# Optimization experiments

Hardware: AMD Instinct MI355X
Metric: run time of the kernel (lower is better)

Reference implementation:

```python
import jax, jax.numpy as jnp
import numpy as np

B, C, L = 8, 256, 2048
D = C // 8  # q/k channel dim = 32


def setup_inputs() -> dict:
    key = jax.random.key(0)
    kx, kq, kk, kv, kg = jax.random.split(key, 5)
    kq1, kq2 = jax.random.split(kq)
    kk1, kk2 = jax.random.split(kk)
    kv1, kv2 = jax.random.split(kv)
    s = 0.05
    return {
        "x": jax.random.normal(kx, (B, C, L), dtype=jnp.float32),
        "Wq": jax.random.normal(kq1, (D, C), dtype=jnp.float32) * s,
        "bq": jax.random.normal(kq2, (D,), dtype=jnp.float32) * s,
        "Wk": jax.random.normal(kk1, (D, C), dtype=jnp.float32) * s,
        "bk": jax.random.normal(kk2, (D,), dtype=jnp.float32) * s,
        "Wv": jax.random.normal(kv1, (C, C), dtype=jnp.float32) * s,
        "bv": jax.random.normal(kv2, (C,), dtype=jnp.float32) * s,
        "gamma": jax.random.normal(kg, (1,), dtype=jnp.float32) * 0.1,
    }


def reference(x, Wq, bq, Wk, bk, Wv, bv, gamma):
    # 1x1 Conv1d == per-position channel matmul
    Q = jnp.einsum("dc,bcl->bld", Wq, x) + bq            # (B, L, D)
    K = jnp.einsum("dc,bcl->bdl", Wk, x) + bk[:, None]   # (B, D, L)
    V = jnp.einsum("oc,bcl->bol", Wv, x) + bv[:, None]   # (B, C, L)
    scale = jnp.float32(1.0 / np.sqrt(D))
    # attn[b, i, j]: softmax over j (keys)
    attn = jax.nn.softmax(jnp.einsum("bid,bdj->bij", Q, K) * scale, axis=-1)
    # out = V @ attn^T : out[b, c, i] = sum_j V[b, c, j] * attn[b, i, j]
    out = jnp.einsum("bcj,bij->bci", V, attn)            # (B, C, L)
    return gamma * out + x
```

## Files before the change

### kernel.cpp

```cpp
#include <hip/hip_runtime.h>
#include <stdint.h>


#define BB 8
#define CC 256
#define LL 2048
#define DD 32

typedef unsigned short u16;
typedef __attribute__((ext_vector_type(8))) short short8;
typedef __attribute__((ext_vector_type(4))) float f32x4;

#define SCALE_LOG2E 0.2550348612f

static __device__ __forceinline__ uint32_t pack2bf16(float hi, float lo) {
    return (__float_as_uint(hi) & 0xFFFF0000u) | (__float_as_uint(lo) >> 16);
}

static __device__ __forceinline__ float fexp2(float v) {
#if __has_builtin(__builtin_amdgcn_exp2f)
    return __builtin_amdgcn_exp2f(v);
#else
    return exp2f(v);
#endif
}

static __device__ __forceinline__ float frcp(float v) {
#if __has_builtin(__builtin_amdgcn_rcpf)
    return __builtin_amdgcn_rcpf(v);
#else
    return 1.0f / v;
#endif
}

__global__ __launch_bounds__(256) void prep_w_kernel(
    const float* __restrict__ Wq, const float* __restrict__ Wk,
    const float* __restrict__ Wv, u16* __restrict__ Wh)
{
    int idx = blockIdx.x * 256 + threadIdx.x;
    int r = idx >> 6;
    int c4 = (idx & 63) << 2;
    const float* src;
    if (r < 32)       src = Wq + (size_t)r * CC + c4;
    else if (r < 64)  src = Wk + (size_t)(r - 32) * CC + c4;
    else              src = Wv + (size_t)(r - 64) * CC + c4;
    float4 v = *(const float4*)src;
    uint2 o;
    o.x = pack2bf16(v.y, v.x);
    o.y = pack2bf16(v.w, v.z);
    *(uint2*)(Wh + (size_t)r * CC + c4) = o;
}

__global__ __launch_bounds__(512, 2) void proj_kernel(
    const float* __restrict__ x, const u16* __restrict__ Wh,
    const float* __restrict__ bq, const float* __restrict__ bk,
    const float* __restrict__ bv,
    u16* __restrict__ Qh, u16* __restrict__ Kth, u16* __restrict__ Vh)
{
    __shared__ u16 xls[32 * 264];
    const int blk = blockIdx.x;
    const int b = blk & 7;
    const int l0 = (blk >> 3) << 5;
    const int tid = threadIdx.x;
    const int w = tid >> 6;
    const int lane = tid & 63;
    const int ln = lane & 15;
    const int q = lane >> 4;

#pragma unroll
    for (int cc = 0; cc < 4; ++cc) {
        const int c = cc * 64 + (tid >> 3);
        const int l4 = (tid & 7) * 4;
        const float4 v = *(const float4*)(x + ((size_t)(b * CC + c)) * LL + l0 + l4);
        xls[(l4 + 0) * 264 + c] = (u16)(__float_as_uint(v.x) >> 16);
        xls[(l4 + 1) * 264 + c] = (u16)(__float_as_uint(v.y) >> 16);
        xls[(l4 + 2) * 264 + c] = (u16)(__float_as_uint(v.z) >> 16);
        xls[(l4 + 3) * 264 + c] = (u16)(__float_as_uint(v.w) >> 16);
    }
    __syncthreads();

    const int wl = w & 1;
    const int wm = w >> 1;
    const int mbase = wm * 80;
    const int l = l0 + wl * 16 + ln;

    f32x4 acc[5];
#pragma unroll
    for (int i = 0; i < 5; ++i) acc[i] = (f32x4){0.f, 0.f, 0.f, 0.f};

#pragma unroll
    for (int c0 = 0; c0 < CC; c0 += 32) {
        const short8 bf = *(const short8*)(&xls[(wl * 16 + ln) * 264 + c0 + q * 8]);
#pragma unroll
        for (int mt = 0; mt < 5; ++mt) {
            const short8 af = *(const short8*)(Wh + (size_t)(mbase + mt * 16 + ln) * CC + c0 + q * 8);
            acc[mt] = __builtin_amdgcn_mfma_f32_16x16x32_bf16(af, bf, acc[mt], 0, 0, 0);
        }
    }

#pragma unroll
    for (int mt = 0; mt < 5; ++mt) {
        const int rg = mbase + mt * 16 + q * 4;
        if (rg < 32) {
            float v0 = (acc[mt][0] + bq[rg + 0]) * SCALE_LOG2E;
            float v1 = (acc[mt][1] + bq[rg + 1]) * SCALE_LOG2E;
            float v2 = (acc[mt][2] + bq[rg + 2]) * SCALE_LOG2E;
            float v3 = (acc[mt][3] + bq[rg + 3]) * SCALE_LOG2E;
            uint2 o; o.x = pack2bf16(v1, v0); o.y = pack2bf16(v3, v2);
            *(uint2*)(Qh + ((size_t)(b * LL) + l) * DD + rg) = o;
        } else if (rg < 64) {
            const int rk = rg - 32;
            float v0 = acc[mt][0] + bk[rk + 0];
            float v1 = acc[mt][1] + bk[rk + 1];
            float v2 = acc[mt][2] + bk[rk + 2];
            float v3 = acc[mt][3] + bk[rk + 3];
            uint2 o; o.x = pack2bf16(v1, v0); o.y = pack2bf16(v3, v2);
            *(uint2*)(Kth + ((size_t)(b * LL) + l) * DD + rk) = o;
        } else {
            const int cv = rg - 64;
#pragma unroll
            for (int rr = 0; rr < 4; ++rr) {
                const float v = acc[mt][rr] + bv[cv + rr];
                Vh[((size_t)(b * CC) + cv + rr) * LL + l] = (u16)(__float_as_uint(v) >> 16);
            }
        }
    }
}

__global__ __launch_bounds__(512, 1) void attn_kernel(
    const u16* __restrict__ Qh, const u16* __restrict__ Kth,
    const u16* __restrict__ Vh, const float* __restrict__ x,
    const float* __restrict__ gamma, float* __restrict__ out)
{
    __shared__ u16 pbuf[8 * 64 * 40];
    __shared__ float obuf[256 * 68];
    __shared__ float lbuf[8 * 64];

    const int blk = blockIdx.x;
    const int b = blk & 7;
    const int i0 = (blk >> 3) << 6;
    const int tid = threadIdx.x;
    const int w = tid >> 6;
    const int wc = w >> 2;
    const int wj = w & 3;
    const int lane = tid & 63;
    const int ln = lane & 15;
    const int q = lane >> 4;

    u16* pb = pbuf + w * (64 * 40);
    const u16* Qb = Qh + ((size_t)(b * LL) + i0) * DD;
    const u16* Kb = Kth + (size_t)(b * LL) * DD;
    const u16* Vb = Vh + ((size_t)(b * CC) + wc * 128) * LL;

    short8 qf[4];
#pragma unroll
    for (int it = 0; it < 4; ++it)
        qf[it] = *(const short8*)(Qb + (size_t)(it * 16 + ln) * DD + q * 8);

    const f32x4 zf = {0.f, 0.f, 0.f, 0.f};
    f32x4 oacc[8][4];
#pragma unroll
    for (int a = 0; a < 8; ++a)
#pragma unroll
        for (int c = 0; c < 4; ++c) oacc[a][c] = zf;
    float lsum[4] = {0.f, 0.f, 0.f, 0.f};

    int jb = wj * 32;
    short8 kf0 = *(const short8*)(Kb + (size_t)(jb + ln) * DD + q * 8);
    short8 kf1 = *(const short8*)(Kb + (size_t)(jb + 16 + ln) * DD + q * 8);

    for (int n = 0; n < 16; ++n) {
        jb = n * 128 + wj * 32;
        const int jnx = (n < 15) ? (n + 1) * 128 + wj * 32 : jb;

        short8 vf[8];
#pragma unroll
        for (int ct = 0; ct < 8; ++ct)
            vf[ct] = *(const short8*)(Vb + (size_t)(ct * 16 + ln) * LL + jb + q * 8);
        const short8 kn0 = *(const short8*)(Kb + (size_t)(jnx + ln) * DD + q * 8);
        const short8 kn1 = *(const short8*)(Kb + (size_t)(jnx + 16 + ln) * DD + q * 8);

#pragma unroll
        for (int jt = 0; jt < 2; ++jt) {
            const short8 kf = jt ? kf1 : kf0;
#pragma unroll
            for (int it = 0; it < 4; ++it) {
                const f32x4 st = __builtin_amdgcn_mfma_f32_16x16x32_bf16(kf, qf[it], zf, 0, 0, 0);
                const float e0 = fexp2(st[0]), e1 = fexp2(st[1]);
                const float e2 = fexp2(st[2]), e3 = fexp2(st[3]);
                lsum[it] += (e0 + e1) + (e2 + e3);
                uint2 d; d.x = pack2bf16(e1, e0); d.y = pack2bf16(e3, e2);
                *(uint2*)(&pb[(it * 16 + ln) * 40 + jt * 16 + q * 4]) = d;
            }
        }

        short8 pf[4];
#pragma unroll
        for (int it = 0; it < 4; ++it)
            pf[it] = *(const short8*)(&pb[(it * 16 + ln) * 40 + q * 8]);

#pragma unroll
        for (int ct = 0; ct < 8; ++ct)
#pragma unroll
            for (int it = 0; it < 4; ++it)
                oacc[ct][it] = __builtin_amdgcn_mfma_f32_16x16x32_bf16(vf[ct], pf[it], oacc[ct][it], 0, 0, 0);

        kf0 = kn0; kf1 = kn1;
    }

#pragma unroll
    for (int it = 0; it < 4; ++it) {
        float s = lsum[it];
        s += __shfl_xor(s, 16);
        s += __shfl_xor(s, 32);
        lsum[it] = s;
    }
    if (q == 0) {
#pragma unroll
        for (int it = 0; it < 4; ++it) lbuf[w * 64 + it * 16 + ln] = lsum[it];
    }

#pragma unroll
    for (int p = 0; p < 4; ++p) {
        if (wj == p) {
#pragma unroll
            for (int ct = 0; ct < 8; ++ct)
#pragma unroll
                for (int it = 0; it < 4; ++it) {
                    const int i = it * 16 + ln;
#pragma unroll
                    for (int r = 0; r < 4; ++r) {
                        const int c = wc * 128 + ct * 16 + q * 4 + r;
                        if (p == 0) obuf[c * 68 + i] = oacc[ct][it][r];
                        else        obuf[c * 68 + i] += oacc[ct][it][r];
                    }
                }
        }
        __syncthreads();
    }

    const float g = gamma[0];
    const int i4 = (tid & 15) * 4;
    float4 sv = {0.f, 0.f, 0.f, 0.f};
#pragma unroll
    for (int ww = 0; ww < 8; ++ww) {
        const float4 lv = *(const float4*)&lbuf[ww * 64 + i4];
        sv.x += lv.x; sv.y += lv.y; sv.z += lv.z; sv.w += lv.w;
    }
    float4 li;
    li.x = 2.0f * frcp(sv.x); li.y = 2.0f * frcp(sv.y);
    li.z = 2.0f * frcp(sv.z); li.w = 2.0f * frcp(sv.w);

#pragma unroll
    for (int cc = 0; cc < 8; ++cc) {
        const int c = cc * 32 + (tid >> 4);
        const float4 ov = *(const float4*)&obuf[c * 68 + i4];
        const size_t idx = ((size_t)(b * CC + c)) * LL + i0 + i4;
        const float4 xv = *(const float4*)(x + idx);
        float4 o;
        o.x = g * (ov.x * li.x) + xv.x;
        o.y = g * (ov.y * li.y) + xv.y;
        o.z = g * (ov.z * li.z) + xv.z;
        o.w = g * (ov.w * li.w) + xv.w;
        *(float4*)(out + idx) = o;
    }
}

extern "C" void kernel_launch(void* const* d_in, const int* in_sizes, int n_in,
                              void* d_out, int out_size, void* d_ws, size_t ws_size,
                              hipStream_t stream)
{
    const float* x     = (const float*)d_in[0];
    const float* Wq    = (const float*)d_in[1];
    const float* bq    = (const float*)d_in[2];
    const float* Wk    = (const float*)d_in[3];
    const float* bk    = (const float*)d_in[4];
    const float* Wv    = (const float*)d_in[5];
    const float* bv    = (const float*)d_in[6];
    const float* gamma = (const float*)d_in[7];
    float* out = (float*)d_out;

    uint8_t* ws = (uint8_t*)d_ws;
    u16* Wh  = (u16*)(ws + 0x000000);
    u16* Qh  = (u16*)(ws + 0x040000);
    u16* Kth = (u16*)(ws + 0x140000);
    u16* Vh  = (u16*)(ws + 0x240000);

    prep_w_kernel<<<80, 256, 0, stream>>>(Wq, Wk, Wv, Wh);
    proj_kernel<<<512, 512, 0, stream>>>(x, Wh, bq, bk, bv, Qh, Kth, Vh);
    attn_kernel<<<256, 512, 0, stream>>>(Qh, Kth, Vh, x, gamma, out);
}
```

Baseline: 149.4 us.

## Retile attention to 128 queries x 128 channels per block; stage V stores via LDS

```diff
diff --git a/kernel.cpp b/kernel.cpp
--- a/kernel.cpp
+++ b/kernel.cpp
@@ -58,6 +58,7 @@
     u16* __restrict__ Qh, u16* __restrict__ Kth, u16* __restrict__ Vh)
 {
     __shared__ u16 xls[32 * 264];
+    __shared__ __attribute__((aligned(16))) u16 vls[256 * 40];
     const int blk = blockIdx.x;
     const int b = blk & 7;
     const int l0 = (blk >> 3) << 5;
@@ -83,6 +84,7 @@
     const int wm = w >> 1;
     const int mbase = wm * 80;
     const int l = l0 + wl * 16 + ln;
+    const int li = wl * 16 + ln;
 
     f32x4 acc[5];
 #pragma unroll
@@ -121,9 +123,21 @@
 #pragma unroll
             for (int rr = 0; rr < 4; ++rr) {
                 const float v = acc[mt][rr] + bv[cv + rr];
-                Vh[((size_t)(b * CC) + cv + rr) * LL + l] = (u16)(__float_as_uint(v) >> 16);
+                vls[(cv + rr) * 40 + li] = (u16)(__float_as_uint(v) >> 16);
             }
         }
+    }
+
+    __syncthreads();
+    {
+        const int row = tid >> 1;
+        const int h = (tid & 1) * 16;
+        const u16* src = &vls[row * 40 + h];
+        const uint4 v0 = *(const uint4*)(src);
+        const uint4 v1 = *(const uint4*)(src + 8);
+        uint4* dst = (uint4*)(Vh + ((size_t)(b * CC) + row) * LL + l0 + h);
+        dst[0] = v0;
+        dst[1] = v1;
     }
 }
 
@@ -132,13 +146,14 @@
     const u16* __restrict__ Vh, const float* __restrict__ x,
     const float* __restrict__ gamma, float* __restrict__ out)
 {
-    __shared__ u16 pbuf[8 * 64 * 40];
-    __shared__ float obuf[256 * 68];
-    __shared__ float lbuf[8 * 64];
+    __shared__ __attribute__((aligned(16))) u16 pbuf[8][128 * 40];
+    __shared__ float obuf[128 * 132];
+    __shared__ float lbuf[8 * 128];
 
     const int blk = blockIdx.x;
     const int b = blk & 7;
-    const int i0 = (blk >> 3) << 6;
+    const int ch = (blk >> 3) & 1;
+    const int i0 = (blk >> 4) << 7;
     const int tid = threadIdx.x;
     const int w = tid >> 6;
     const int wc = w >> 2;
@@ -147,35 +162,34 @@
     const int ln = lane & 15;
     const int q = lane >> 4;
 
-    u16* pb = pbuf + w * (64 * 40);
+    u16* pb = &pbuf[w][0];
     const u16* Qb = Qh + ((size_t)(b * LL) + i0) * DD;
     const u16* Kb = Kth + (size_t)(b * LL) * DD;
-    const u16* Vb = Vh + ((size_t)(b * CC) + wc * 128) * LL;
-
-    short8 qf[4];
-#pragma unroll
-    for (int it = 0; it < 4; ++it)
+    const u16* Vb = Vh + ((size_t)(b * CC) + ch * 128 + wc * 64) * LL;
+
+    short8 qf[8];
+#pragma unroll
+    for (int it = 0; it < 8; ++it)
         qf[it] = *(const short8*)(Qb + (size_t)(it * 16 + ln) * DD + q * 8);
 
     const f32x4 zf = {0.f, 0.f, 0.f, 0.f};
-    f32x4 oacc[8][4];
-#pragma unroll
-    for (int a = 0; a < 8; ++a)
-#pragma unroll
-        for (int c = 0; c < 4; ++c) oacc[a][c] = zf;
-    float lsum[4] = {0.f, 0.f, 0.f, 0.f};
-
-    int jb = wj * 32;
-    short8 kf0 = *(const short8*)(Kb + (size_t)(jb + ln) * DD + q * 8);
-    short8 kf1 = *(const short8*)(Kb + (size_t)(jb + 16 + ln) * DD + q * 8);
+    f32x4 oacc[4][8];
+#pragma unroll
+    for (int a = 0; a < 4; ++a)
+#pragma unroll
+        for (int c = 0; c < 8; ++c) oacc[a][c] = zf;
+    float lsum[8] = {0.f, 0.f, 0.f, 0.f, 0.f, 0.f, 0.f, 0.f};
+
+    short8 kf0 = *(const short8*)(Kb + (size_t)(wj * 32 + ln) * DD + q * 8);
+    short8 kf1 = *(const short8*)(Kb + (size_t)(wj * 32 + 16 + ln) * DD + q * 8);
 
     for (int n = 0; n < 16; ++n) {
-        jb = n * 128 + wj * 32;
+        const int jb = n * 128 + wj * 32;
         const int jnx = (n < 15) ? (n + 1) * 128 + wj * 32 : jb;
 
-        short8 vf[8];
-#pragma unroll
-        for (int ct = 0; ct < 8; ++ct)
+        short8 vf[4];
+#pragma unroll
+        for (int ct = 0; ct < 4; ++ct)
             vf[ct] = *(const short8*)(Vb + (size_t)(ct * 16 + ln) * LL + jb + q * 8);
         const short8 kn0 = *(const short8*)(Kb + (size_t)(jnx + ln) * DD + q * 8);
         const short8 kn1 = *(const short8*)(Kb + (size_t)(jnx + 16 + ln) * DD + q * 8);
@@ -184,7 +198,7 @@
         for (int jt = 0; jt < 2; ++jt) {
             const short8 kf = jt ? kf1 : kf0;
 #pragma unroll
-            for (int it = 0; it < 4; ++it) {
+            for (int it = 0; it < 8; ++it) {
                 const f32x4 st = __builtin_amdgcn_mfma_f32_16x16x32_bf16(kf, qf[it], zf, 0, 0, 0);
                 const float e0 = fexp2(st[0]), e1 = fexp2(st[1]);
                 const float e2 = fexp2(st[2]), e3 = fexp2(st[3]);
@@ -194,22 +208,25 @@
             }
         }
 
-        short8 pf[4];
-#pragma unroll
-        for (int it = 0; it < 4; ++it)
-            pf[it] = *(const short8*)(&pb[(it * 16 + ln) * 40 + q * 8]);
-
-#pragma unroll
-        for (int ct = 0; ct < 8; ++ct)
+#pragma unroll
+        for (int ih = 0; ih < 2; ++ih) {
+            short8 pf[4];
 #pragma unroll
             for (int it = 0; it < 4; ++it)
-                oacc[ct][it] = __builtin_amdgcn_mfma_f32_16x16x32_bf16(vf[ct], pf[it], oacc[ct][it], 0, 0, 0);
+                pf[it] = *(const short8*)(&pb[((ih * 4 + it) * 16 + ln) * 40 + q * 8]);
+#pragma unroll
+            for (int ct = 0; ct < 4; ++ct)
+#pragma unroll
+                for (int it = 0; it < 4; ++it)
+                    oacc[ct][ih * 4 + it] = __builtin_amdgcn_mfma_f32_16x16x32_bf16(
+                        vf[ct], pf[it], oacc[ct][ih * 4 + it], 0, 0, 0);
+        }
 
         kf0 = kn0; kf1 = kn1;
     }
 
 #pragma unroll
-    for (int it = 0; it < 4; ++it) {
+    for (int it = 0; it < 8; ++it) {
         float s = lsum[it];
         s += __shfl_xor(s, 16);
         s += __shfl_xor(s, 32);
@@ -217,22 +234,22 @@
     }
     if (q == 0) {
 #pragma unroll
-        for (int it = 0; it < 4; ++it) lbuf[w * 64 + it * 16 + ln] = lsum[it];
+        for (int it = 0; it < 8; ++it) lbuf[w * 128 + it * 16 + ln] = lsum[it];
     }
 
 #pragma unroll
     for (int p = 0; p < 4; ++p) {
         if (wj == p) {
 #pragma unroll
-            for (int ct = 0; ct < 8; ++ct)
-#pragma unroll
-                for (int it = 0; it < 4; ++it) {
+            for (int ct = 0; ct < 4; ++ct)
+#pragma unroll
+                for (int it = 0; it < 8; ++it) {
                     const int i = it * 16 + ln;
 #pragma unroll
                     for (int r = 0; r < 4; ++r) {
-                        const int c = wc * 128 + ct * 16 + q * 4 + r;
-                        if (p == 0) obuf[c * 68 + i] = oacc[ct][it][r];
-                        else        obuf[c * 68 + i] += oacc[ct][it][r];
+                        const int c = wc * 64 + ct * 16 + q * 4 + r;
+                        if (p == 0) obuf[c * 132 + i] = oacc[ct][it][r];
+                        else        obuf[c * 132 + i] += oacc[ct][it][r];
                     }
                 }
         }
@@ -240,11 +257,12 @@
     }
 
     const float g = gamma[0];
-    const int i4 = (tid & 15) * 4;
+    const int i4 = (tid & 31) * 4;
+    const int crow = tid >> 5;
     float4 sv = {0.f, 0.f, 0.f, 0.f};
 #pragma unroll
     for (int ww = 0; ww < 8; ++ww) {
-        const float4 lv = *(const float4*)&lbuf[ww * 64 + i4];
+        const float4 lv = *(const float4*)&lbuf[ww * 128 + i4];
         sv.x += lv.x; sv.y += lv.y; sv.z += lv.z; sv.w += lv.w;
     }
     float4 li;
@@ -253,9 +271,9 @@
 
 #pragma unroll
     for (int cc = 0; cc < 8; ++cc) {
-        const int c = cc * 32 + (tid >> 4);
-        const float4 ov = *(const float4*)&obuf[c * 68 + i4];
-        const size_t idx = ((size_t)(b * CC + c)) * LL + i0 + i4;
+        const int c = cc * 16 + crow;
+        const float4 ov = *(const float4*)&obuf[c * 132 + i4];
+        const size_t idx = ((size_t)(b * CC + ch * 128 + c)) * LL + i0 + i4;
         const float4 xv = *(const float4*)(x + idx);
         float4 o;
         o.x = g * (ov.x * li.x) + xv.x;
```

Result: slower. 179.7 us (+20.3%).

## Retile projection kernel to 64-position tiles split by output half, stage V via LDS

Applied to the files above, without the earlier changes.

```diff
diff --git a/kernel.cpp b/kernel.cpp
--- a/kernel.cpp
+++ b/kernel.cpp
@@ -57,72 +57,98 @@
     const float* __restrict__ bv,
     u16* __restrict__ Qh, u16* __restrict__ Kth, u16* __restrict__ Vh)
 {
-    __shared__ u16 xls[32 * 264];
+    __shared__ u16 xls[64 * 264];
+    __shared__ __attribute__((aligned(16))) u16 vls[160 * 72];
     const int blk = blockIdx.x;
-    const int b = blk & 7;
-    const int l0 = (blk >> 3) << 5;
+    const int b  = blk & 7;
+    const int l0 = ((blk >> 3) & 31) << 6;
+    const int mh = blk >> 8;
     const int tid = threadIdx.x;
     const int w = tid >> 6;
     const int lane = tid & 63;
     const int ln = lane & 15;
     const int q = lane >> 4;
 
-#pragma unroll
-    for (int cc = 0; cc < 4; ++cc) {
-        const int c = cc * 64 + (tid >> 3);
-        const int l4 = (tid & 7) * 4;
-        const float4 v = *(const float4*)(x + ((size_t)(b * CC + c)) * LL + l0 + l4);
-        xls[(l4 + 0) * 264 + c] = (u16)(__float_as_uint(v.x) >> 16);
-        xls[(l4 + 1) * 264 + c] = (u16)(__float_as_uint(v.y) >> 16);
-        xls[(l4 + 2) * 264 + c] = (u16)(__float_as_uint(v.z) >> 16);
-        xls[(l4 + 3) * 264 + c] = (u16)(__float_as_uint(v.w) >> 16);
+    {
+        const int c = tid >> 1;
+        const int lh32 = (tid & 1) * 32;
+        const float* xp = x + ((size_t)(b * CC + c)) * LL + l0 + lh32;
+#pragma unroll
+        for (int k4 = 0; k4 < 8; ++k4) {
+            const float4 v = *(const float4*)(xp + k4 * 4);
+            const int l = lh32 + k4 * 4;
+            xls[(l + 0) * 264 + c] = (u16)(__float_as_uint(v.x) >> 16);
+            xls[(l + 1) * 264 + c] = (u16)(__float_as_uint(v.y) >> 16);
+            xls[(l + 2) * 264 + c] = (u16)(__float_as_uint(v.z) >> 16);
+            xls[(l + 3) * 264 + c] = (u16)(__float_as_uint(v.w) >> 16);
+        }
     }
     __syncthreads();
 
-    const int wl = w & 1;
     const int wm = w >> 1;
-    const int mbase = wm * 80;
-    const int l = l0 + wl * 16 + ln;
-
-    f32x4 acc[5];
-#pragma unroll
-    for (int i = 0; i < 5; ++i) acc[i] = (f32x4){0.f, 0.f, 0.f, 0.f};
+    const int lh = w & 1;
+    const int mbase = mh * 160 + wm * 80;
+
+    f32x4 acc[5][2];
+#pragma unroll
+    for (int i = 0; i < 5; ++i)
+#pragma unroll
+        for (int j = 0; j < 2; ++j) acc[i][j] = (f32x4){0.f, 0.f, 0.f, 0.f};
 
 #pragma unroll
     for (int c0 = 0; c0 < CC; c0 += 32) {
-        const short8 bf = *(const short8*)(&xls[(wl * 16 + ln) * 264 + c0 + q * 8]);
+        const short8 bf0 = *(const short8*)(&xls[(lh * 32 + ln) * 264 + c0 + q * 8]);
+        const short8 bf1 = *(const short8*)(&xls[(lh * 32 + 16 + ln) * 264 + c0 + q * 8]);
 #pragma unroll
         for (int mt = 0; mt < 5; ++mt) {
             const short8 af = *(const short8*)(Wh + (size_t)(mbase + mt * 16 + ln) * CC + c0 + q * 8);
-            acc[mt] = __builtin_amdgcn_mfma_f32_16x16x32_bf16(af, bf, acc[mt], 0, 0, 0);
-        }
-    }
-
+            acc[mt][0] = __builtin_amdgcn_mfma_f32_16x16x32_bf16(af, bf0, acc[mt][0], 0, 0, 0);
+            acc[mt][1] = __builtin_amdgcn_mfma_f32_16x16x32_bf16(af, bf1, acc[mt][1], 0, 0, 0);
+        }
+    }
+
+    const int vbase = mh ? 96 : 0;
 #pragma unroll
     for (int mt = 0; mt < 5; ++mt) {
         const int rg = mbase + mt * 16 + q * 4;
-        if (rg < 32) {
-            float v0 = (acc[mt][0] + bq[rg + 0]) * SCALE_LOG2E;
-            float v1 = (acc[mt][1] + bq[rg + 1]) * SCALE_LOG2E;
-            float v2 = (acc[mt][2] + bq[rg + 2]) * SCALE_LOG2E;
-            float v3 = (acc[mt][3] + bq[rg + 3]) * SCALE_LOG2E;
-            uint2 o; o.x = pack2bf16(v1, v0); o.y = pack2bf16(v3, v2);
-            *(uint2*)(Qh + ((size_t)(b * LL) + l) * DD + rg) = o;
-        } else if (rg < 64) {
-            const int rk = rg - 32;
-            float v0 = acc[mt][0] + bk[rk + 0];
-            float v1 = acc[mt][1] + bk[rk + 1];
-            float v2 = acc[mt][2] + bk[rk + 2];
-            float v3 = acc[mt][3] + bk[rk + 3];
-            uint2 o; o.x = pack2bf16(v1, v0); o.y = pack2bf16(v3, v2);
-            *(uint2*)(Kth + ((size_t)(b * LL) + l) * DD + rk) = o;
-        } else {
-            const int cv = rg - 64;
-#pragma unroll
-            for (int rr = 0; rr < 4; ++rr) {
-                const float v = acc[mt][rr] + bv[cv + rr];
-                Vh[((size_t)(b * CC) + cv + rr) * LL + l] = (u16)(__float_as_uint(v) >> 16);
+#pragma unroll
+        for (int lx = 0; lx < 2; ++lx) {
+            const int l = l0 + lh * 32 + lx * 16 + ln;
+            if (rg < 32) {
+                float v0 = (acc[mt][lx][0] + bq[rg + 0]) * SCALE_LOG2E;
+                float v1 = (acc[mt][lx][1] + bq[rg + 1]) * SCALE_LOG2E;
+                float v2 = (acc[mt][lx][2] + bq[rg + 2]) * SCALE_LOG2E;
+                float v3 = (acc[mt][lx][3] + bq[rg + 3]) * SCALE_LOG2E;
+                uint2 o; o.x = pack2bf16(v1, v0); o.y = pack2bf16(v3, v2);
+                *(uint2*)(Qh + ((size_t)(b * LL) + l) * DD + rg) = o;
+            } else if (rg < 64) {
+                const int rk = rg - 32;
+                float v0 = acc[mt][lx][0] + bk[rk + 0];
+                float v1 = acc[mt][lx][1] + bk[rk + 1];
+                float v2 = acc[mt][lx][2] + bk[rk + 2];
+                float v3 = acc[mt][lx][3] + bk[rk + 3];
+                uint2 o; o.x = pack2bf16(v1, v0); o.y = pack2bf16(v3, v2);
+                *(uint2*)(Kth + ((size_t)(b * LL) + l) * DD + rk) = o;
+            } else {
+                const int cv = rg - 64;
+                const int cl = cv - vbase;
+#pragma unroll
+                for (int rr = 0; rr < 4; ++rr) {
+                    const float v = acc[mt][lx][rr] + bv[cv + rr];
+                    vls[(cl + rr) * 72 + lh * 32 + lx * 16 + ln] = (u16)(__float_as_uint(v) >> 16);
+                }
             }
+        }
+    }
+
+    __syncthreads();
+    {
+        const int R = mh ? 160 : 96;
+        for (int idx = tid; idx < R * 8; idx += 512) {
+            const int row = idx >> 3;
+            const int h = (idx & 7) * 8;
+            const uint4 v = *(const uint4*)(&vls[row * 72 + h]);
+            *(uint4*)(Vh + ((size_t)(b * CC) + vbase + row) * LL + l0 + h) = v;
         }
     }
 }
```

Result: slower. 153.5 us (+2.8%).
